# Kernel tuning notes

Measured on AMD Instinct MI355X. Metric: run time of the kernel, lower is better.

Reference implementation:

```python
import jax, jax.numpy as jnp
import numpy as np

L, B, N, IN, H, ATTN, RED, OUT = 3, 8, 512, 64, 128, 32, 32, 3


def setup_inputs() -> dict:
    key = jax.random.key(0)
    ks = jax.random.split(key, 34)
    def rn(i, shape, s=0.05):
        return jax.random.normal(ks[i], shape, dtype=jnp.float32) * s
    inp = {
        "X": rn(0, (B, N, IN), 1.0),
        # sparse binary adjacency (avg degree ~10) and denser clique graph
        "A": (jax.random.uniform(ks[1], (B, N, N)) < 0.02).astype(jnp.float32),
        "Ac": (jax.random.uniform(ks[2], (B, N, N)) < 0.05).astype(jnp.float32),
        # topo embedding
        "embed_w": rn(3, (H, IN)), "embed_b": jnp.zeros((H,), jnp.float32),
        "topo_eps": jnp.zeros((1,), jnp.float32),
        "topo_w": rn(4, (H, H)), "topo_b": jnp.zeros((H,), jnp.float32),
        "theta": rn(5, (H, 2)),
        # per-layer dual GIN (index 0: A, index 1: Ac)
        "gin_eps": jnp.zeros((L, 2, 1), jnp.float32),
        "gin_w": rn(6, (L, 2, H, H)), "gin_b": jnp.zeros((L, 2, H), jnp.float32),
        # per-layer flexible attention
        "wo": rn(7, (L, ATTN, H)), "w1": rn(8, (L, ATTN, H)),
        "wphi": rn(9, (L, ATTN)),
        "wy_w": rn(10, (L, H, H)), "wy_b": jnp.zeros((L, H), jnp.float32),
        "we_w": rn(11, (L, H, ATTN)), "we_b": jnp.zeros((L, H), jnp.float32),
        # per-layer SE block
        "lin1_w": rn(12, (L, RED, H)), "lin1_b": jnp.zeros((L, RED), jnp.float32),
        "lin2_w": rn(13, (L, H, RED)), "lin2_b": jnp.zeros((L, H), jnp.float32),
        "mlp_w": rn(14, (L, H, H)), "mlp_b": jnp.zeros((L, H), jnp.float32),
        # node head
        "head1_w": rn(15, (H // 2, H)), "head1_b": jnp.zeros((H // 2,), jnp.float32),
        "head2_w": rn(16, (OUT, H // 2)), "head2_b": jnp.zeros((OUT,), jnp.float32),
    }
    return inp


def _lin(x, w, b=None):
    y = x @ w.T
    return y if b is None else y + b


def _gin(x, a, eps, w, b):
    # (1+eps)*X + A@X, then Linear, then ReLU
    return jax.nn.relu(_lin((1.0 + eps) * x + a @ x, w, b))


def _forward(X, A, Ac, embed_w, embed_b, topo_eps, topo_w, topo_b, theta,
             gin_eps, gin_w, gin_b, wo, w1, wphi, wy_w, wy_b, we_w, we_b,
             lin1_w, lin1_b, lin2_w, lin2_b, mlp_w, mlp_b,
             head1_w, head1_b, head2_w, head2_b):
    # TopoPositionalEmbedding (shared GIN on both graphs)
    Xh = _lin(X, embed_w, embed_b)                      # (B,N,H)
    hA = _gin(Xh, A, topo_eps[0], topo_w, topo_b)
    hAC = _gin(Xh, Ac, topo_eps[0], topo_w, topo_b)
    Xp = Xh + jnp.tanh(hA * theta[:, 0]) + jnp.tanh(hAC * theta[:, 1])

    for l in range(L):
        # dual GIN
        XA = _gin(Xp, A, gin_eps[l, 0, 0], gin_w[l, 0], gin_b[l, 0])
        XAC = _gin(Xp, Ac, gin_eps[l, 1, 0], gin_w[l, 1], gin_b[l, 1])
        # GRIT-style flexible attention
        ho = Xp @ wo[l].T                               # (B,N,ATTN)
        h1 = Xp @ w1[l].T
        e = jnp.tanh(ho[:, :, None, :] + h1[:, None, :, :])   # (B,N,N,ATTN)
        alpha = jax.nn.softmax(e @ wphi[l], axis=-1)    # (B,N,N)
        Xy = _lin(Xp, wy_w[l], wy_b[l])                 # (B,N,H)
        # sum_j alpha_ij * We(e_ij) == We(sum_j alpha_ij * e_ij) since We is affine
        # and sum_j alpha_ij == 1 (avoids the (B,N,N,H) intermediate)
        ctx = jnp.einsum('bij,bijd->bid', alpha, e)     # (B,N,ATTN)
        Xatt = alpha @ Xy + _lin(ctx, we_w[l], we_b[l])
        Xbar = XA + XAC + Xatt
        # SE gating
        y1 = jax.nn.relu(_lin(Xbar.sum(axis=1), lin1_w[l], lin1_b[l]))
        y2 = jax.nn.sigmoid(_lin(y1, lin2_w[l], lin2_b[l]))
        Xp = _lin(Xbar * y2[:, None, :], mlp_w[l], mlp_b[l])

    h = jax.nn.relu(_lin(Xp, head1_w, head1_b))
    return _lin(h, head2_w, head2_b)                    # (B,N,OUT)


def reference(X, A, Ac, embed_w, embed_b, topo_eps, topo_w, topo_b, theta,
              gin_eps, gin_w, gin_b, wo, w1, wphi, wy_w, wy_b, we_w, we_b,
              lin1_w, lin1_b, lin2_w, lin2_b, mlp_w, mlp_b,
              head1_w, head1_b, head2_w, head2_b):
    return _forward(X, A, Ac, embed_w, embed_b, topo_eps, topo_w, topo_b, theta,
                    gin_eps, gin_w, gin_b, wo, w1, wphi, wy_w, wy_b, we_w, we_b,
                    lin1_w, lin1_b, lin2_w, lin2_b, mlp_w, mlp_b,
                    head1_w, head1_b, head2_w, head2_b)
```

## Files before the change

kernel.cpp:

```cpp
#include <hip/hip_runtime.h>

#define Bc 8
#define Nc 512
#define INc 64
#define Hc 128
#define Atc 32
#define REDc 32
#define OUTc 3
#define Lc 3
#define MNc (Bc * Nc)
#define KT 32
#define WPAD 36

__device__ __forceinline__ float tanh_fast(float x) {
    float e = __expf(2.f * x);
    return 1.f - 2.f * __builtin_amdgcn_rcpf(e + 1.f);
}

__global__ __launch_bounds__(256) void prologue(
        const float* __restrict__ A, const float* __restrict__ Acg,
        int* __restrict__ idxA, int* __restrict__ idxC,
        int* __restrict__ cntA, int* __restrict__ cntC,
        const float* __restrict__ X, const float* __restrict__ embed_w,
        const float* __restrict__ embed_b, float* __restrict__ Xh) {
    __shared__ int cA, cC;
    __shared__ float xs[8 * INc];
    int blk = blockIdx.x;
    int t = threadIdx.x;
    if (blk < MNc) {
        if (t == 0) { cA = 0; cC = 0; }
        __syncthreads();
        if (t < 128) {
            int h = t;
            int* ia = idxA + (size_t)blk * Nc;
            int* ic = idxC + (size_t)blk * Nc;
            float4 a4 = ((const float4*)(A + (size_t)blk * Nc))[h];
            if (a4.x != 0.f) ia[atomicAdd(&cA, 1)] = 4 * h;
            if (a4.y != 0.f) ia[atomicAdd(&cA, 1)] = 4 * h + 1;
            if (a4.z != 0.f) ia[atomicAdd(&cA, 1)] = 4 * h + 2;
            if (a4.w != 0.f) ia[atomicAdd(&cA, 1)] = 4 * h + 3;
            float4 c4 = ((const float4*)(Acg + (size_t)blk * Nc))[h];
            if (c4.x != 0.f) ic[atomicAdd(&cC, 1)] = 4 * h;
            if (c4.y != 0.f) ic[atomicAdd(&cC, 1)] = 4 * h + 1;
            if (c4.z != 0.f) ic[atomicAdd(&cC, 1)] = 4 * h + 2;
            if (c4.w != 0.f) ic[atomicAdd(&cC, 1)] = 4 * h + 3;
        }
        __syncthreads();
        if (t == 0) { cntA[blk] = cA; cntC[blk] = cC; }
    } else {
        int m0 = (blk - MNc) * 8;
        if (t < 128) ((float4*)xs)[t] = ((const float4*)(X + (size_t)m0 * INc))[t];
        __syncthreads();
        int n = t & 127, grp = t >> 7;
        float bv = embed_b[n];
        float acc[4];
#pragma unroll
        for (int r = 0; r < 4; ++r) acc[r] = bv;
        const float* w = embed_w + (size_t)n * INc;
        for (int k = 0; k < INc; k += 4) {
            float4 wv = *(const float4*)(w + k);
#pragma unroll
            for (int r = 0; r < 4; ++r) {
                float4 xv = *(const float4*)(xs + (grp * 4 + r) * INc + k);
                acc[r] = fmaf(xv.x, wv.x, acc[r]); acc[r] = fmaf(xv.y, wv.y, acc[r]);
                acc[r] = fmaf(xv.z, wv.z, acc[r]); acc[r] = fmaf(xv.w, wv.w, acc[r]);
            }
        }
#pragma unroll
        for (int r = 0; r < 4; ++r)
            Xh[(size_t)(m0 + grp * 4 + r) * Hc + n] = acc[r];
    }
}

__global__ __launch_bounds__(128) void spmm_pre(
        const int* __restrict__ idxA, const int* __restrict__ idxC,
        const int* __restrict__ cntA, const int* __restrict__ cntC,
        const float* __restrict__ X, const float* __restrict__ eA,
        const float* __restrict__ eC, float* __restrict__ T1, float* __restrict__ T2) {
    int bi = blockIdx.x;
    int b = bi >> 9;
    int h = threadIdx.x;
    __shared__ int ias[Nc], ics[Nc];
    int nA = cntA[bi], nC = cntC[bi];
    for (int q = h; q < nA; q += 128) ias[q] = idxA[(size_t)bi * Nc + q];
    for (int q = h; q < nC; q += 128) ics[q] = idxC[(size_t)bi * Nc + q];
    __syncthreads();
    const float* Xb = X + (size_t)b * Nc * Hc;
    float a1 = 0.f, a2 = 0.f;
    for (int q = 0; q < nA; ++q) a1 += Xb[(size_t)ias[q] * Hc + h];
    for (int q = 0; q < nC; ++q) a2 += Xb[(size_t)ics[q] * Hc + h];
    size_t o = (size_t)bi * Hc + h;
    float xv = X[o];
    T1[o] = (1.f + eA[0]) * xv + a1;
    T2[o] = (1.f + eC[0]) * xv + a2;
}

__global__ __launch_bounds__(256) void gemm2_topo(
        const float* __restrict__ T1, const float* __restrict__ T2,
        const float* __restrict__ W, const float* __restrict__ bias,
        const float* __restrict__ Xh, const float* __restrict__ theta,
        float* __restrict__ Xp) {
    __shared__ float xs1[8 * Hc], xs2[8 * Hc];
    int m0 = blockIdx.x * 8;
    int t = threadIdx.x;
    for (int idx4 = t; idx4 < 8 * Hc / 4; idx4 += 256) {
        ((float4*)xs1)[idx4] = ((const float4*)(T1 + (size_t)m0 * Hc))[idx4];
        ((float4*)xs2)[idx4] = ((const float4*)(T2 + (size_t)m0 * Hc))[idx4];
    }
    __syncthreads();
    int n = t & 127, grp = t >> 7;
    float bv = bias[n];
    float ac1[4], ac2[4];
#pragma unroll
    for (int r = 0; r < 4; ++r) { ac1[r] = bv; ac2[r] = bv; }
    const float* w = W + (size_t)n * Hc;
    for (int k = 0; k < Hc; k += 4) {
        float4 wv = *(const float4*)(w + k);
#pragma unroll
        for (int r = 0; r < 4; ++r) {
            float4 x1 = *(const float4*)(xs1 + (grp * 4 + r) * Hc + k);
            float4 x2 = *(const float4*)(xs2 + (grp * 4 + r) * Hc + k);
            ac1[r] = fmaf(x1.x, wv.x, ac1[r]); ac1[r] = fmaf(x1.y, wv.y, ac1[r]);
            ac1[r] = fmaf(x1.z, wv.z, ac1[r]); ac1[r] = fmaf(x1.w, wv.w, ac1[r]);
            ac2[r] = fmaf(x2.x, wv.x, ac2[r]); ac2[r] = fmaf(x2.y, wv.y, ac2[r]);
            ac2[r] = fmaf(x2.z, wv.z, ac2[r]); ac2[r] = fmaf(x2.w, wv.w, ac2[r]);
        }
    }
    float th0 = theta[2 * n], th1 = theta[2 * n + 1];
#pragma unroll
    for (int r = 0; r < 4; ++r) {
        size_t o = (size_t)(m0 + grp * 4 + r) * Hc + n;
        float g1 = fmaxf(ac1[r], 0.f), g2 = fmaxf(ac2[r], 0.f);
        Xp[o] = Xh[o] + tanh_fast(g1 * th0) + tanh_fast(g2 * th1);
    }
}

__device__ __forceinline__ void stage_wtile(
        const float* __restrict__ W, int kt, float* Ws, int t) {
#pragma unroll
    for (int i = 0; i < 4; ++i) {
        int idx = t + i * 256;
        int row = idx >> 3, c4 = idx & 7;
        float4 v = *(const float4*)(W + (size_t)row * Hc + kt + c4 * 4);
        *(float4*)(Ws + row * WPAD + c4 * 4) = v;
    }
}

__device__ __forceinline__ void gemm_lds(
        const float* __restrict__ W, const float* xsrc, float* Ws,
        int n, int grp, int t, float acc[4]) {
#pragma unroll 1
    for (int kt = 0; kt < Hc; kt += KT) {
        __syncthreads();
        stage_wtile(W, kt, Ws, t);
        __syncthreads();
#pragma unroll
        for (int k = 0; k < KT; k += 4) {
            float4 wv = *(const float4*)(Ws + n * WPAD + k);
#pragma unroll
            for (int r = 0; r < 4; ++r) {
                float4 xv = *(const float4*)(xsrc + (grp * 4 + r) * Hc + kt + k);
                acc[r] = fmaf(xv.x, wv.x, acc[r]); acc[r] = fmaf(xv.y, wv.y, acc[r]);
                acc[r] = fmaf(xv.z, wv.z, acc[r]); acc[r] = fmaf(xv.w, wv.w, acc[r]);
            }
        }
    }
}

__global__ __launch_bounds__(256) void layer_gemms(
        const float* __restrict__ T1, const float* __restrict__ T2,
        const float* __restrict__ W1, const float* __restrict__ b1,
        const float* __restrict__ W2, const float* __restrict__ b2,
        const float* __restrict__ Xp, const float* __restrict__ wy_w,
        const float* __restrict__ wy_b, const float* __restrict__ wo,
        const float* __restrict__ w1a, float* __restrict__ GS,
        float* __restrict__ Xy, float* __restrict__ hov, float* __restrict__ h1v) {
    __shared__ float xs1[8 * Hc], xs2[8 * Hc], xs[8 * Hc];
    __shared__ float Ws[Hc * WPAD];
    int m0 = blockIdx.x * 8;
    int t = threadIdx.x;
    for (int idx4 = t; idx4 < 8 * Hc / 4; idx4 += 256) {
        ((float4*)xs1)[idx4] = ((const float4*)(T1 + (size_t)m0 * Hc))[idx4];
        ((float4*)xs2)[idx4] = ((const float4*)(T2 + (size_t)m0 * Hc))[idx4];
        ((float4*)xs)[idx4]  = ((const float4*)(Xp + (size_t)m0 * Hc))[idx4];
    }
    int n = t & 127, grp = t >> 7;
    {
        float ac1[4], ac2[4];
        float bv1 = b1[n], bv2 = b2[n];
#pragma unroll
        for (int r = 0; r < 4; ++r) { ac1[r] = bv1; ac2[r] = bv2; }
        gemm_lds(W1, xs1, Ws, n, grp, t, ac1);
        gemm_lds(W2, xs2, Ws, n, grp, t, ac2);
#pragma unroll
        for (int r = 0; r < 4; ++r) {
            size_t o = (size_t)(m0 + grp * 4 + r) * Hc + n;
            GS[o] = fmaxf(ac1[r], 0.f) + fmaxf(ac2[r], 0.f);
        }
    }
    {
        float bv = wy_b[n];
        float acc[4];
#pragma unroll
        for (int r = 0; r < 4; ++r) acc[r] = bv;
        gemm_lds(wy_w, xs, Ws, n, grp, t, acc);
#pragma unroll
        for (int r = 0; r < 4; ++r)
            Xy[(size_t)(m0 + grp * 4 + r) * Hc + n] = acc[r];
    }
    {
        int n2 = t & 63, g2 = t >> 6;
        const float* w = (n2 < 32) ? (wo + (size_t)n2 * Hc) : (w1a + (size_t)(n2 - 32) * Hc);
        float acc[2] = {0.f, 0.f};
        for (int k = 0; k < Hc; k += 4) {
            float4 wv = *(const float4*)(w + k);
#pragma unroll
            for (int r = 0; r < 2; ++r) {
                float4 xv = *(const float4*)(xs + (g2 * 2 + r) * Hc + k);
                acc[r] = fmaf(xv.x, wv.x, acc[r]); acc[r] = fmaf(xv.y, wv.y, acc[r]);
                acc[r] = fmaf(xv.z, wv.z, acc[r]); acc[r] = fmaf(xv.w, wv.w, acc[r]);
            }
        }
#pragma unroll
        for (int r = 0; r < 2; ++r) {
            int m = m0 + g2 * 2 + r;
            float v = tanh_fast(acc[r]);
            if (n2 < 32) hov[(size_t)m * Atc + n2] = v;
            else h1v[(size_t)m * Atc + (n2 - 32)] = v;
        }
    }
}

__global__ __launch_bounds__(256, 4) void attn_part(
        const float* __restrict__ ta, const float* __restrict__ tb,
        const float* __restrict__ wphi, const float* __restrict__ Xy,
        float* __restrict__ Pp, float* __restrict__ ctxp, float* __restrict__ wsp) {
    int blk = blockIdx.x;
    int b = blk >> 8;
    int r6 = (blk >> 2) & 63;
    int js = blk & 3;
    int i0 = r6 * 8;
    int t = threadIdx.x;
    __shared__ float als[8 * 128];
    __shared__ float4 red4[1024];
    __shared__ float tas[8 * 32];
    tas[t] = ta[((size_t)b * Nc + i0) * 32 + t];
    __syncthreads();
    {
        int i = t >> 5;
        int kq = t & 3;
        int jl = (t >> 2) & 7;
        float4 wp0 = ((const float4*)wphi)[kq * 2];
        float4 wp1 = ((const float4*)wphi)[kq * 2 + 1];
        float4 ta0 = *(const float4*)(tas + i * 32 + kq * 8);
        float4 ta1 = *(const float4*)(tas + i * 32 + kq * 8 + 4);
        const float* tbb = tb + ((size_t)b * Nc + js * 128) * 32;
        const float4* p = (const float4*)(tbb + (size_t)jl * 32 + kq * 8);
        float4 c0a = p[0], c0b = p[1];
        float4 c1a = p[64], c1b = p[65];
        float ca[8];
#pragma unroll
        for (int q = 0; q < 8; ++q) ca[q] = 0.f;
        float wsum = 0.f;
#pragma unroll 4
        for (int jj = 0; jj < 16; ++jj) {
            float4 ha = c0a, hb = c0b;
            c0a = c1a; c0b = c1b;
            if (jj < 14) { c1a = p[(jj + 2) * 64]; c1b = p[(jj + 2) * 64 + 1]; }
            float e0 = (ta0.x + ha.x) * __builtin_amdgcn_rcpf(fmaf(ta0.x, ha.x, 1.f));
            float e1 = (ta0.y + ha.y) * __builtin_amdgcn_rcpf(fmaf(ta0.y, ha.y, 1.f));
            float e2 = (ta0.z + ha.z) * __builtin_amdgcn_rcpf(fmaf(ta0.z, ha.z, 1.f));
            float e3 = (ta0.w + ha.w) * __builtin_amdgcn_rcpf(fmaf(ta0.w, ha.w, 1.f));
            float e4 = (ta1.x + hb.x) * __builtin_amdgcn_rcpf(fmaf(ta1.x, hb.x, 1.f));
            float e5 = (ta1.y + hb.y) * __builtin_amdgcn_rcpf(fmaf(ta1.y, hb.y, 1.f));
            float e6 = (ta1.z + hb.z) * __builtin_amdgcn_rcpf(fmaf(ta1.z, hb.z, 1.f));
            float e7 = (ta1.w + hb.w) * __builtin_amdgcn_rcpf(fmaf(ta1.w, hb.w, 1.f));
            float s01 = fmaf(e1, wp0.y, e0 * wp0.x);
            float s23 = fmaf(e3, wp0.w, e2 * wp0.z);
            float s45 = fmaf(e5, wp1.y, e4 * wp1.x);
            float s67 = fmaf(e7, wp1.w, e6 * wp1.z);
            float sc = (s01 + s23) + (s45 + s67);
            sc += __shfl_xor(sc, 1);
            sc += __shfl_xor(sc, 2);
            float w = __expf(sc);
            if (kq == 0) als[i * 128 + jj * 8 + jl] = w;
            wsum += w;
            ca[0] = fmaf(w, e0, ca[0]);
            ca[1] = fmaf(w, e1, ca[1]);
            ca[2] = fmaf(w, e2, ca[2]);
            ca[3] = fmaf(w, e3, ca[3]);
            ca[4] = fmaf(w, e4, ca[4]);
            ca[5] = fmaf(w, e5, ca[5]);
            ca[6] = fmaf(w, e6, ca[6]);
            ca[7] = fmaf(w, e7, ca[7]);
        }
#pragma unroll
        for (int o = 16; o > 0; o >>= 1) wsum += __shfl_xor(wsum, o);
        if ((t & 31) == 0) wsp[(size_t)js * MNc + (size_t)b * Nc + i0 + i] = wsum;
#pragma unroll
        for (int q = 0; q < 8; ++q) {
            ca[q] += __shfl_xor(ca[q], 4);
            ca[q] += __shfl_xor(ca[q], 8);
            ca[q] += __shfl_xor(ca[q], 16);
        }
        if (jl == 0) {
            float* cp = ctxp + ((size_t)js * MNc + (size_t)b * Nc + i0 + i) * 32 + kq * 8;
#pragma unroll
            for (int q = 0; q < 8; ++q) cp[q] = ca[q];
        }
    }
    __syncthreads();
    {
        int h4 = t & 31, jg = t >> 5;
        const float* xp = Xy + (((size_t)b * Nc + js * 128) + jg * 16) * Hc + h4 * 4;
        float* Pb = Pp + (size_t)js * MNc * Hc;
        float4 acc[8];
#pragma unroll
        for (int r = 0; r < 8; ++r) acc[r] = make_float4(0.f, 0.f, 0.f, 0.f);
        float4 xc = *(const float4*)(xp);
        float4 xn = *(const float4*)(xp + Hc);
#pragma unroll 4
        for (int jq = 0; jq < 16; ++jq) {
            float4 x = xc;
            xc = xn;
            if (jq < 14) xn = *(const float4*)(xp + (jq + 2) * Hc);
            int j = jg * 16 + jq;
#pragma unroll
            for (int r = 0; r < 8; ++r) {
                float av = als[r * 128 + j];
                acc[r].x = fmaf(av, x.x, acc[r].x);
                acc[r].y = fmaf(av, x.y, acc[r].y);
                acc[r].z = fmaf(av, x.z, acc[r].z);
                acc[r].w = fmaf(av, x.w, acc[r].w);
            }
        }
#pragma unroll
        for (int r = 0; r < 4; ++r) red4[jg * 128 + r * 32 + h4] = acc[r];
        __syncthreads();
        if (t < 128) {
            int ii = t >> 5, hq = t & 31;
            float4 s = red4[ii * 32 + hq];
#pragma unroll
            for (int gq = 1; gq < 8; ++gq) {
                float4 p = red4[gq * 128 + ii * 32 + hq];
                s.x += p.x; s.y += p.y; s.z += p.z; s.w += p.w;
            }
            *(float4*)(Pb + ((size_t)b * Nc + i0 + ii) * Hc + hq * 4) = s;
        }
        __syncthreads();
#pragma unroll
        for (int r = 0; r < 4; ++r) red4[jg * 128 + r * 32 + h4] = acc[4 + r];
        __syncthreads();
        if (t < 128) {
            int ii = t >> 5, hq = t & 31;
            float4 s = red4[ii * 32 + hq];
#pragma unroll
            for (int gq = 1; gq < 8; ++gq) {
                float4 p = red4[gq * 128 + ii * 32 + hq];
                s.x += p.x; s.y += p.y; s.z += p.z; s.w += p.w;
            }
            *(float4*)(Pb + ((size_t)b * Nc + i0 + 4 + ii) * Hc + hq * 4) = s;
        }
    }
}

__global__ __launch_bounds__(256) void combine_se(
        const float* __restrict__ Pp, const float* __restrict__ ctxp,
        const float* __restrict__ wsp, const float* __restrict__ we_w,
        const float* __restrict__ we_b, const float* __restrict__ GS,
        float* __restrict__ Xbar, float* __restrict__ part) {
    int blk = blockIdx.x;
    int m0 = blk * 8;
    int t = threadIdx.x;
    __shared__ float ctxs[8 * 32];
    __shared__ float sinv[8];
    __shared__ float4 sred[256];
    if (t < 8) {
        float ws = 0.f;
#pragma unroll
        for (int s = 0; s < 4; ++s) ws += wsp[(size_t)s * MNc + m0 + t];
        sinv[t] = 4.f / ws;
    }
    {
        float c = 0.f;
#pragma unroll
        for (int s = 0; s < 4; ++s) c += ctxp[((size_t)s * MNc + m0) * 32 + t];
        ctxs[t] = c;
    }
    __syncthreads();
    int ii = t >> 5, hq = t & 31;
    size_t o = (size_t)(m0 + ii) * Hc + hq * 4;
    float4 ps = *(const float4*)(Pp + o);
#pragma unroll
    for (int s = 1; s < 4; ++s) {
        float4 p = *(const float4*)(Pp + (size_t)s * MNc * Hc + o);
        ps.x += p.x; ps.y += p.y; ps.z += p.z; ps.w += p.w;
    }
    float si = sinv[ii];
    const float* c = ctxs + ii * 32;
    float wec[4];
#pragma unroll
    for (int ho_ = 0; ho_ < 4; ++ho_) {
        const float4* wrow = (const float4*)(we_w + (size_t)(hq * 4 + ho_) * 32);
        float sv = 0.f;
#pragma unroll
        for (int q = 0; q < 8; ++q) {
            float4 w4 = wrow[q];
            sv = fmaf(w4.x, c[4 * q], sv); sv = fmaf(w4.y, c[4 * q + 1], sv);
            sv = fmaf(w4.z, c[4 * q + 2], sv); sv = fmaf(w4.w, c[4 * q + 3], sv);
        }
        wec[ho_] = sv;
    }
    float4 wb = *(const float4*)(we_b + hq * 4);
    float4 gv = *(const float4*)(GS + o);
    float4 outv;
    outv.x = (ps.x + wec[0]) * si + wb.x + gv.x;
    outv.y = (ps.y + wec[1]) * si + wb.y + gv.y;
    outv.z = (ps.z + wec[2]) * si + wb.z + gv.z;
    outv.w = (ps.w + wec[3]) * si + wb.w + gv.w;
    *(float4*)(Xbar + o) = outv;
    sred[ii * 32 + hq] = outv;
    __syncthreads();
    if (t < 32) {
        float4 s0 = sred[t];
#pragma unroll
        for (int g = 1; g < 8; ++g) {
            float4 p = sred[g * 32 + t];
            s0.x += p.x; s0.y += p.y; s0.z += p.z; s0.w += p.w;
        }
        *(float4*)(part + (size_t)blk * Hc + t * 4) = s0;
    }
}

template <int LAST>
__global__ __launch_bounds__(256) void mlp_gemm(
        const float* __restrict__ Xbar, const float* __restrict__ W,
        const float* __restrict__ bias, const float* __restrict__ part,
        const float* __restrict__ l1w, const float* __restrict__ l1b,
        const float* __restrict__ l2w, const float* __restrict__ l2b,
        float* __restrict__ Y,
        const float* __restrict__ h1w, const float* __restrict__ h1b,
        const float* __restrict__ h2w, const float* __restrict__ h2b,
        float* __restrict__ out) {
    __shared__ float xs[8 * Hc];
    __shared__ float s[Hc];
    __shared__ float y1s[REDc];
    __shared__ float y2s[Hc];
    __shared__ float hs[8 * 64];
    __shared__ float Ws[Hc * WPAD];
    int m0 = blockIdx.x * 8;
    int b = m0 >> 9;
    int t = threadIdx.x;
    ((float4*)xs)[t] = ((const float4*)(Xbar + (size_t)m0 * Hc))[t];
    if (t < 128) {
        const float* pb = part + (size_t)b * 64 * Hc;
        float acc = 0.f;
        for (int p = 0; p < 64; ++p) acc += pb[p * Hc + t];
        s[t] = acc;
    }
    __syncthreads();
    if (t < REDc) {
        float a = l1b[t];
        const float* w = l1w + (size_t)t * Hc;
        for (int k = 0; k < Hc; ++k) a = fmaf(s[k], w[k], a);
        y1s[t] = fmaxf(a, 0.f);
    }
    __syncthreads();
    if (t < 128) {
        float a = l2b[t];
        const float* w2 = l2w + (size_t)t * REDc;
#pragma unroll
        for (int k = 0; k < REDc; ++k) a = fmaf(y1s[k], w2[k], a);
        y2s[t] = 1.f / (1.f + __expf(-a));
    }
    __syncthreads();
    {
        float4 yv = ((const float4*)y2s)[t & 31];
        float4 v = ((float4*)xs)[t];
        v.x *= yv.x; v.y *= yv.y; v.z *= yv.z; v.w *= yv.w;
        ((float4*)xs)[t] = v;
    }
    int n = t & 127, grp = t >> 7;
    float bv = bias[n];
    float acc[4];
#pragma unroll
    for (int r = 0; r < 4; ++r) acc[r] = bv;
    gemm_lds(W, xs, Ws, n, grp, t, acc);
    if (!LAST) {
#pragma unroll
        for (int r = 0; r < 4; ++r)
            Y[(size_t)(m0 + grp * 4 + r) * Hc + n] = acc[r];
    } else {
        __syncthreads();
#pragma unroll
        for (int r = 0; r < 4; ++r) xs[(grp * 4 + r) * Hc + n] = acc[r];
        __syncthreads();
        {
            int n2 = t & 63, g2 = t >> 6;
            float a0 = h1b[n2], a1 = a0;
            const float* wh = h1w + (size_t)n2 * Hc;
            const float* x0 = xs + (g2 * 2) * Hc;
            const float* x1 = xs + (g2 * 2 + 1) * Hc;
            for (int k = 0; k < Hc; k += 4) {
                float4 wv = *(const float4*)(wh + k);
                float4 v0 = *(const float4*)(x0 + k);
                float4 v1 = *(const float4*)(x1 + k);
                a0 = fmaf(v0.x, wv.x, a0); a0 = fmaf(v0.y, wv.y, a0);
                a0 = fmaf(v0.z, wv.z, a0); a0 = fmaf(v0.w, wv.w, a0);
                a1 = fmaf(v1.x, wv.x, a1); a1 = fmaf(v1.y, wv.y, a1);
                a1 = fmaf(v1.z, wv.z, a1); a1 = fmaf(v1.w, wv.w, a1);
            }
            hs[(g2 * 2) * 64 + n2] = fmaxf(a0, 0.f);
            hs[(g2 * 2 + 1) * 64 + n2] = fmaxf(a1, 0.f);
        }
        __syncthreads();
        if (t < 8 * OUTc) {
            int m = t / OUTc, o = t - m * OUTc;
            float a = h2b[o];
            const float* w2 = h2w + (size_t)o * 64;
            const float* hr = hs + m * 64;
#pragma unroll
            for (int k = 0; k < 64; ++k) a = fmaf(hr[k], w2[k], a);
            out[(size_t)(m0 + m) * OUTc + o] = a;
        }
    }
}

extern "C" void kernel_launch(void* const* d_in, const int* in_sizes, int n_in,
                              void* d_out, int out_size, void* d_ws, size_t ws_size,
                              hipStream_t stream) {
    const float* X       = (const float*)d_in[0];
    const float* A       = (const float*)d_in[1];
    const float* Acg     = (const float*)d_in[2];
    const float* embed_w = (const float*)d_in[3];
    const float* embed_b = (const float*)d_in[4];
    const float* topo_eps= (const float*)d_in[5];
    const float* topo_w  = (const float*)d_in[6];
    const float* topo_b  = (const float*)d_in[7];
    const float* theta   = (const float*)d_in[8];
    const float* gin_eps = (const float*)d_in[9];
    const float* gin_w   = (const float*)d_in[10];
    const float* gin_b   = (const float*)d_in[11];
    const float* wo      = (const float*)d_in[12];
    const float* w1      = (const float*)d_in[13];
    const float* wphi    = (const float*)d_in[14];
    const float* wy_w    = (const float*)d_in[15];
    const float* wy_b    = (const float*)d_in[16];
    const float* we_w    = (const float*)d_in[17];
    const float* we_b    = (const float*)d_in[18];
    const float* lin1_w  = (const float*)d_in[19];
    const float* lin1_b  = (const float*)d_in[20];
    const float* lin2_w  = (const float*)d_in[21];
    const float* lin2_b  = (const float*)d_in[22];
    const float* mlp_w   = (const float*)d_in[23];
    const float* mlp_b   = (const float*)d_in[24];
    const float* head1_w = (const float*)d_in[25];
    const float* head1_b = (const float*)d_in[26];
    const float* head2_w = (const float*)d_in[27];
    const float* head2_b = (const float*)d_in[28];
    float* out = (float*)d_out;

    float* ws = (float*)d_ws;
    const int MN = Bc * Nc;
    const size_t SZ = (size_t)MN * Hc;
    float* Xh   = ws;
    float* Xp   = Xh + SZ;
    float* T1   = Xp + SZ;
    float* T2   = T1 + SZ;
    float* GS   = T2 + SZ;
    float* Xy   = GS + SZ;
    float* hov  = Xy + SZ;
    float* h1v  = hov + (size_t)MN * Atc;
    float* part = h1v + (size_t)MN * Atc;
    float* Pp   = part + (size_t)(MN / 8) * Hc;
    float* ctxp = Pp + 4 * SZ;
    float* wsp  = ctxp + (size_t)4 * MN * Atc;
    int* idxA   = (int*)(wsp + (size_t)4 * MN);
    int* idxC   = idxA + (size_t)MN * Nc;
    int* cntA   = idxC + (size_t)MN * Nc;
    int* cntC   = cntA + MN;
    float* Xbar = T1;

    prologue<<<MN + MN / 8, 256, 0, stream>>>(A, Acg, idxA, idxC, cntA, cntC,
                                              X, embed_w, embed_b, Xh);
    spmm_pre<<<MN, 128, 0, stream>>>(idxA, idxC, cntA, cntC, Xh, topo_eps, topo_eps, T1, T2);
    gemm2_topo<<<MN / 8, 256, 0, stream>>>(T1, T2, topo_w, topo_b, Xh, theta, Xp);

    for (int l = 0; l < Lc; ++l) {
        spmm_pre<<<MN, 128, 0, stream>>>(idxA, idxC, cntA, cntC, Xp,
                                         gin_eps + l * 2, gin_eps + l * 2 + 1, T1, T2);
        layer_gemms<<<MN / 8, 256, 0, stream>>>(T1, T2,
            gin_w + (size_t)(l * 2 + 0) * Hc * Hc, gin_b + (size_t)(l * 2 + 0) * Hc,
            gin_w + (size_t)(l * 2 + 1) * Hc * Hc, gin_b + (size_t)(l * 2 + 1) * Hc,
            Xp, wy_w + (size_t)l * Hc * Hc, wy_b + (size_t)l * Hc,
            wo + (size_t)l * Atc * Hc, w1 + (size_t)l * Atc * Hc,
            GS, Xy, hov, h1v);
        attn_part<<<MN / 2, 256, 0, stream>>>(hov, h1v, wphi + (size_t)l * Atc, Xy,
                                              Pp, ctxp, wsp);
        combine_se<<<MN / 8, 256, 0, stream>>>(Pp, ctxp, wsp,
                                               we_w + (size_t)l * Hc * Atc,
                                               we_b + (size_t)l * Hc, GS, Xbar, part);
        if (l < Lc - 1) {
            mlp_gemm<0><<<MN / 8, 256, 0, stream>>>(Xbar, mlp_w + (size_t)l * Hc * Hc,
                mlp_b + (size_t)l * Hc, part,
                lin1_w + (size_t)l * REDc * Hc, lin1_b + (size_t)l * REDc,
                lin2_w + (size_t)l * Hc * REDc, lin2_b + (size_t)l * Hc,
                Xp, head1_w, head1_b, head2_w, head2_b, out);
        } else {
            mlp_gemm<1><<<MN / 8, 256, 0, stream>>>(Xbar, mlp_w + (size_t)l * Hc * Hc,
                mlp_b + (size_t)l * Hc, part,
                lin1_w + (size_t)l * REDc * Hc, lin1_b + (size_t)l * REDc,
                lin2_w + (size_t)l * Hc * REDc, lin2_b + (size_t)l * Hc,
                Xp, head1_w, head1_b, head2_w, head2_b, out);
        }
    }
}
```

Before: 438.2 us.

## Split layer GEMMs into role-specialized blocks with 32-row register-tiled GEMM

Replaces the per-8-row fused kernel that ran three GEMMs sequentially with blocks that each handle one role (GIN-A, GIN-C, Wy, or attention projections) over 32 rows. Uses a 4x4 register tile so each staged weight tile is reused across more rows, cutting weight staging and LDS traffic per output. GIN outputs are now written to two separate buffers and summed in combine_se, adding an extra read stream and workspace. The attention-projection role does less work than the others, so the blocks are load-imbalanced.

```diff
diff --git a/kernel.cpp b/kernel.cpp
--- a/kernel.cpp
+++ b/kernel.cpp
@@ -167,67 +167,108 @@
     }
 }
 
-__global__ __launch_bounds__(256) void layer_gemms(
+__global__ __launch_bounds__(256) void layer_gemm4(
         const float* __restrict__ T1, const float* __restrict__ T2,
         const float* __restrict__ W1, const float* __restrict__ b1,
         const float* __restrict__ W2, const float* __restrict__ b2,
         const float* __restrict__ Xp, const float* __restrict__ wy_w,
         const float* __restrict__ wy_b, const float* __restrict__ wo,
-        const float* __restrict__ w1a, float* __restrict__ GS,
-        float* __restrict__ Xy, float* __restrict__ hov, float* __restrict__ h1v) {
-    __shared__ float xs1[8 * Hc], xs2[8 * Hc], xs[8 * Hc];
+        const float* __restrict__ w1a, float* __restrict__ GS1,
+        float* __restrict__ GS2, float* __restrict__ Xy,
+        float* __restrict__ hov, float* __restrict__ h1v) {
+    __shared__ float xs[32 * Hc];
     __shared__ float Ws[Hc * WPAD];
-    int m0 = blockIdx.x * 8;
+    int blk = blockIdx.x;
+    int role = blk >> 7;
+    int m0 = (blk & 127) * 32;
     int t = threadIdx.x;
-    for (int idx4 = t; idx4 < 8 * Hc / 4; idx4 += 256) {
-        ((float4*)xs1)[idx4] = ((const float4*)(T1 + (size_t)m0 * Hc))[idx4];
-        ((float4*)xs2)[idx4] = ((const float4*)(T2 + (size_t)m0 * Hc))[idx4];
-        ((float4*)xs)[idx4]  = ((const float4*)(Xp + (size_t)m0 * Hc))[idx4];
-    }
-    int n = t & 127, grp = t >> 7;
+    const float* xsrc = (role == 0) ? T1 : (role == 1) ? T2 : Xp;
     {
-        float ac1[4], ac2[4];
-        float bv1 = b1[n], bv2 = b2[n];
-#pragma unroll
-        for (int r = 0; r < 4; ++r) { ac1[r] = bv1; ac2[r] = bv2; }
-        gemm_lds(W1, xs1, Ws, n, grp, t, ac1);
-        gemm_lds(W2, xs2, Ws, n, grp, t, ac2);
-#pragma unroll
-        for (int r = 0; r < 4; ++r) {
-            size_t o = (size_t)(m0 + grp * 4 + r) * Hc + n;
-            GS[o] = fmaxf(ac1[r], 0.f) + fmaxf(ac2[r], 0.f);
-        }
-    }
-    {
-        float bv = wy_b[n];
-        float acc[4];
-#pragma unroll
-        for (int r = 0; r < 4; ++r) acc[r] = bv;
-        gemm_lds(wy_w, xs, Ws, n, grp, t, acc);
-#pragma unroll
-        for (int r = 0; r < 4; ++r)
-            Xy[(size_t)(m0 + grp * 4 + r) * Hc + n] = acc[r];
-    }
-    {
+        const float4* src = (const float4*)(xsrc + (size_t)m0 * Hc);
+#pragma unroll
+        for (int i = 0; i < 4; ++i) ((float4*)xs)[t + i * 256] = src[t + i * 256];
+    }
+    if (role == 3) {
+        __syncthreads();
         int n2 = t & 63, g2 = t >> 6;
         const float* w = (n2 < 32) ? (wo + (size_t)n2 * Hc) : (w1a + (size_t)(n2 - 32) * Hc);
-        float acc[2] = {0.f, 0.f};
+        float acc[8];
+#pragma unroll
+        for (int r = 0; r < 8; ++r) acc[r] = 0.f;
         for (int k = 0; k < Hc; k += 4) {
             float4 wv = *(const float4*)(w + k);
 #pragma unroll
-            for (int r = 0; r < 2; ++r) {
-                float4 xv = *(const float4*)(xs + (g2 * 2 + r) * Hc + k);
+            for (int r = 0; r < 8; ++r) {
+                float4 xv = *(const float4*)(xs + (g2 * 8 + r) * Hc + k);
                 acc[r] = fmaf(xv.x, wv.x, acc[r]); acc[r] = fmaf(xv.y, wv.y, acc[r]);
                 acc[r] = fmaf(xv.z, wv.z, acc[r]); acc[r] = fmaf(xv.w, wv.w, acc[r]);
             }
         }
 #pragma unroll
-        for (int r = 0; r < 2; ++r) {
-            int m = m0 + g2 * 2 + r;
+        for (int r = 0; r < 8; ++r) {
+            int m = m0 + g2 * 8 + r;
             float v = tanh_fast(acc[r]);
             if (n2 < 32) hov[(size_t)m * Atc + n2] = v;
             else h1v[(size_t)m * Atc + (n2 - 32)] = v;
         }
+        return;
+    }
+    const float* W = (role == 0) ? W1 : (role == 1) ? W2 : wy_w;
+    const float* bias = (role == 0) ? b1 : (role == 1) ? b2 : wy_b;
+    int cg = t & 31, rg = t >> 5;
+    float acc[4][4];
+#pragma unroll
+    for (int r = 0; r < 4; ++r)
+#pragma unroll
+        for (int c = 0; c < 4; ++c) acc[r][c] = 0.f;
+#pragma unroll 1
+    for (int kt = 0; kt < Hc; kt += KT) {
+        __syncthreads();
+        stage_wtile(W, kt, Ws, t);
+        __syncthreads();
+#pragma unroll
+        for (int k = 0; k < KT; k += 4) {
+            float4 xv[4], wv[4];
+#pragma unroll
+            for (int r = 0; r < 4; ++r)
+                xv[r] = *(const float4*)(xs + (rg * 4 + r) * Hc + kt + k);
+#pragma unroll
+            for (int c = 0; c < 4; ++c)
+                wv[c] = *(const float4*)(Ws + (cg + 32 * c) * WPAD + k);
+#pragma unroll
+            for (int r = 0; r < 4; ++r)
+#pragma unroll
+                for (int c = 0; c < 4; ++c) {
+                    acc[r][c] = fmaf(xv[r].x, wv[c].x, acc[r][c]);
+                    acc[r][c] = fmaf(xv[r].y, wv[c].y, acc[r][c]);
+                    acc[r][c] = fmaf(xv[r].z, wv[c].z, acc[r][c]);
+                    acc[r][c] = fmaf(xv[r].w, wv[c].w, acc[r][c]);
+                }
+        }
+    }
+    float bvv[4];
+#pragma unroll
+    for (int c = 0; c < 4; ++c) bvv[c] = bias[cg + 32 * c];
+    if (role == 0) {
+#pragma unroll
+        for (int r = 0; r < 4; ++r)
+#pragma unroll
+            for (int c = 0; c < 4; ++c)
+                GS1[(size_t)(m0 + rg * 4 + r) * Hc + cg + 32 * c] =
+                    fmaxf(acc[r][c] + bvv[c], 0.f);
+    } else if (role == 1) {
+#pragma unroll
+        for (int r = 0; r < 4; ++r)
+#pragma unroll
+            for (int c = 0; c < 4; ++c)
+                GS2[(size_t)(m0 + rg * 4 + r) * Hc + cg + 32 * c] =
+                    fmaxf(acc[r][c] + bvv[c], 0.f);
+    } else {
+#pragma unroll
+        for (int r = 0; r < 4; ++r)
+#pragma unroll
+            for (int c = 0; c < 4; ++c)
+                Xy[(size_t)(m0 + rg * 4 + r) * Hc + cg + 32 * c] = acc[r][c] + bvv[c];
     }
 }
 
@@ -367,7 +408,8 @@
 __global__ __launch_bounds__(256) void combine_se(
         const float* __restrict__ Pp, const float* __restrict__ ctxp,
         const float* __restrict__ wsp, const float* __restrict__ we_w,
-        const float* __restrict__ we_b, const float* __restrict__ GS,
+        const float* __restrict__ we_b, const float* __restrict__ GS1,
+        const float* __restrict__ GS2,
         float* __restrict__ Xbar, float* __restrict__ part) {
     int blk = blockIdx.x;
     int m0 = blk * 8;
@@ -412,12 +454,13 @@
         wec[ho_] = sv;
     }
     float4 wb = *(const float4*)(we_b + hq * 4);
-    float4 gv = *(const float4*)(GS + o);
+    float4 g1 = *(const float4*)(GS1 + o);
+    float4 g2 = *(const float4*)(GS2 + o);
     float4 outv;
-    outv.x = (ps.x + wec[0]) * si + wb.x + gv.x;
-    outv.y = (ps.y + wec[1]) * si + wb.y + gv.y;
-    outv.z = (ps.z + wec[2]) * si + wb.z + gv.z;
-    outv.w = (ps.w + wec[3]) * si + wb.w + gv.w;
+    outv.x = (ps.x + wec[0]) * si + wb.x + g1.x + g2.x;
+    outv.y = (ps.y + wec[1]) * si + wb.y + g1.y + g2.y;
+    outv.z = (ps.z + wec[2]) * si + wb.z + g1.z + g2.z;
+    outv.w = (ps.w + wec[3]) * si + wb.w + g1.w + g2.w;
     *(float4*)(Xbar + o) = outv;
     sred[ii * 32 + hq] = outv;
     __syncthreads();
@@ -567,8 +610,9 @@
     float* Xp   = Xh + SZ;
     float* T1   = Xp + SZ;
     float* T2   = T1 + SZ;
-    float* GS   = T2 + SZ;
-    float* Xy   = GS + SZ;
+    float* GS1  = T2 + SZ;
+    float* GS2  = GS1 + SZ;
+    float* Xy   = GS2 + SZ;
     float* hov  = Xy + SZ;
     float* h1v  = hov + (size_t)MN * Atc;
     float* part = h1v + (size_t)MN * Atc;
@@ -589,17 +633,17 @@
     for (int l = 0; l < Lc; ++l) {
         spmm_pre<<<MN, 128, 0, stream>>>(idxA, idxC, cntA, cntC, Xp,
                                          gin_eps + l * 2, gin_eps + l * 2 + 1, T1, T2);
-        layer_gemms<<<MN / 8, 256, 0, stream>>>(T1, T2,
+        layer_gemm4<<<4 * (MN / 32), 256, 0, stream>>>(T1, T2,
             gin_w + (size_t)(l * 2 + 0) * Hc * Hc, gin_b + (size_t)(l * 2 + 0) * Hc,
             gin_w + (size_t)(l * 2 + 1) * Hc * Hc, gin_b + (size_t)(l * 2 + 1) * Hc,
             Xp, wy_w + (size_t)l * Hc * Hc, wy_b + (size_t)l * Hc,
             wo + (size_t)l * Atc * Hc, w1 + (size_t)l * Atc * Hc,
-            GS, Xy, hov, h1v);
+            GS1, GS2, Xy, hov, h1v);
         attn_part<<<MN / 2, 256, 0, stream>>>(hov, h1v, wphi + (size_t)l * Atc, Xy,
                                               Pp, ctxp, wsp);
         combine_se<<<MN / 8, 256, 0, stream>>>(Pp, ctxp, wsp,
                                                we_w + (size_t)l * Hc * Atc,
-                                               we_b + (size_t)l * Hc, GS, Xbar, part);
+                                               we_b + (size_t)l * Hc, GS1, GS2, Xbar, part);
         if (l < Lc - 1) {
             mlp_gemm<0><<<MN / 8, 256, 0, stream>>>(Xbar, mlp_w + (size_t)l * Hc * Hc,
                 mlp_b + (size_t)l * Hc, part,
```

Measured after the change: 376.2 us, median of 2. 1.16x faster.
